# Optimization experiments

Measured on AMD Instinct MI355X. Metric: run time of the kernel, lower is better.

The kernel has to match this reference:

```python
import jax, jax.numpy as jnp
import numpy as np
import math

D_MODEL = 1024
N_HEADS = 16
HEAD_DIM = D_MODEL // N_HEADS


def get_slopes(n_heads: int) -> jnp.ndarray:
    def pow2_slopes(n):
        start = 2.0 ** (-8.0 / n)
        return np.array([start * start ** i for i in range(n)], dtype=np.float32)
    if math.log2(n_heads).is_integer():
        return jnp.asarray(pow2_slopes(n_heads))
    closest = 2 ** math.floor(math.log2(n_heads))
    base = pow2_slopes(closest)
    extra = pow2_slopes(2 * closest)[::2][: n_heads - closest]
    return jnp.asarray(np.concatenate([base, extra]))


def setup_inputs() -> dict:
    key = jax.random.key(0)
    ks = jax.random.split(key, 9)
    s = 1.0 / math.sqrt(D_MODEL)
    x = jax.random.normal(ks[0], (2, 2048, D_MODEL), dtype=jnp.float32)
    q_w = jax.random.uniform(ks[1], (D_MODEL, D_MODEL), jnp.float32, -s, s)
    q_b = jax.random.uniform(ks[2], (D_MODEL,), jnp.float32, -s, s)
    k_w = jax.random.uniform(ks[3], (D_MODEL, D_MODEL), jnp.float32, -s, s)
    k_b = jax.random.uniform(ks[4], (D_MODEL,), jnp.float32, -s, s)
    v_w = jax.random.uniform(ks[5], (D_MODEL, D_MODEL), jnp.float32, -s, s)
    v_b = jax.random.uniform(ks[6], (D_MODEL,), jnp.float32, -s, s)
    o_w = jax.random.uniform(ks[7], (D_MODEL, D_MODEL), jnp.float32, -s, s)
    o_b = jax.random.uniform(ks[8], (D_MODEL,), jnp.float32, -s, s)
    return {"x": x, "q_w": q_w, "q_b": q_b, "k_w": k_w, "k_b": k_b,
            "v_w": v_w, "v_b": v_b, "o_w": o_w, "o_b": o_b}


def reference(x, q_w, q_b, k_w, k_b, v_w, v_b, o_w, o_b):
    B, S, D = x.shape
    H, hd = N_HEADS, HEAD_DIM
    # torch Linear: y = x @ W.T + b
    Q = (x @ q_w.T + q_b).reshape(B, S, H, hd).transpose(0, 2, 1, 3)  # [B,H,S,hd]
    K = (x @ k_w.T + k_b).reshape(B, S, H, hd).transpose(0, 2, 1, 3)
    V = (x @ v_w.T + v_b).reshape(B, S, H, hd).transpose(0, 2, 1, 3)
    scores = jnp.einsum('bhqd,bhkd->bhqk', Q, K) / math.sqrt(hd)
    # ALiBi bias: slopes[h] * (k_pos - q_pos)
    pos = jnp.arange(S)
    rel = (pos[None, :] - pos[:, None]).astype(scores.dtype)  # [S,S]
    slopes = get_slopes(H)
    scores = scores + slopes[None, :, None, None] * rel[None, None, :, :]
    # causal mask
    causal = pos[None, :] <= pos[:, None]  # [S,S] True where allowed
    scores = jnp.where(causal[None, None], scores, -jnp.inf)
    attn = jax.nn.softmax(scores, axis=-1)  # dropout=0 (eval)
    out = jnp.einsum('bhqk,bhkd->bhqd', attn, V)
    out = out.transpose(0, 2, 1, 3).reshape(B, S, D)
    return out @ o_w.T + o_b
```

## Files before the change

### kernel.cpp

```cpp
#include <hip/hip_runtime.h>

typedef __attribute__((ext_vector_type(8))) short short8;
typedef __attribute__((ext_vector_type(4))) float float4v;
typedef __attribute__((ext_vector_type(4))) short short4v;

#define B_ 2
#define S_ 2048
#define D_ 1024
#define H_ 16
#define HD_ 64
#define M_ 4096
#define LOG2E 1.442695040888963f

__device__ __forceinline__ unsigned short f2bf(float f) {
  unsigned int u = __builtin_bit_cast(unsigned int, f);
  u += 0x7fffu + ((u >> 16) & 1u);
  return (unsigned short)(u >> 16);
}

__device__ __forceinline__ void gload_lds16(const void* g, void* l) {
  __builtin_amdgcn_global_load_lds(
      (const __attribute__((address_space(1))) void*)g,
      (__attribute__((address_space(3))) void*)l, 16, 0, 0);
}

__global__ __launch_bounds__(256, 4) void cvt_kernel(
    const float* __restrict__ x,  const float* __restrict__ qw,
    const float* __restrict__ kw, const float* __restrict__ vw,
    const float* __restrict__ ow, unsigned short* __restrict__ dst)
{
  const int seg = blockIdx.y;
  const float* src;
  size_t doff;
  if (seg < 4)       { src = x + (size_t)seg * 1048576; doff = (size_t)seg * 1048576; }
  else if (seg == 4) { src = qw; doff = 4194304u; }
  else if (seg == 5) { src = kw; doff = 4194304u + 1048576u; }
  else if (seg == 6) { src = vw; doff = 4194304u + 2097152u; }
  else               { src = ow; doff = 4194304u + 3145728u; }
  const size_t i = ((size_t)blockIdx.x * 256 + threadIdx.x) * 4;
  float4v v = *(const float4v*)(src + i);
  short4v p;
#pragma unroll
  for (int r = 0; r < 4; ++r) p[r] = (short)f2bf(v[r]);
  *(short4v*)(dst + doff + i) = p;
}

__global__ __launch_bounds__(256, 2) void gemm_kernel(
    const unsigned short* __restrict__ X,
    const unsigned short* __restrict__ W0, const unsigned short* __restrict__ W1,
    const unsigned short* __restrict__ W2,
    const float* __restrict__ Bi0, const float* __restrict__ Bi1,
    const float* __restrict__ Bi2,
    unsigned short* O0, unsigned short* O1, unsigned short* O2,
    float* OutF, int md0, int md1, int md2)
{
  const int z = blockIdx.z;
  const unsigned short* W  = (z == 0) ? W0  : ((z == 1) ? W1  : W2);
  const float* Bi          = (z == 0) ? Bi0 : ((z == 1) ? Bi1 : Bi2);
  unsigned short* Out      = (z == 0) ? O0  : ((z == 1) ? O1  : O2);
  const int mode           = (z == 0) ? md0 : ((z == 1) ? md1 : md2);

  __shared__ __align__(16) char smem[128 * 32 * 2 * 2];
  char* As = smem;
  char* Bs = smem + 128 * 32 * 2;

  const int t = threadIdx.x, l = t & 63;
  const int w = t >> 6, lr = l & 15, lg = l >> 4;
  const int n0 = blockIdx.x * 128, m0 = blockIdx.y * 128;
  const int wm = (w >> 1) * 64, wn = (w & 1) * 64;

  float4v acc[4][4];
#pragma unroll
  for (int i = 0; i < 4; ++i)
#pragma unroll
    for (int j = 0; j < 4; ++j) acc[i][j] = (float4v){0.f, 0.f, 0.f, 0.f};

  const int c0 = t, c1 = t + 256;
  const int r0 = c0 >> 2, k80 = (c0 & 3) * 8;
  const int r1 = c1 >> 2, k81 = (c1 & 3) * 8;

  for (int k0 = 0; k0 < 1024; k0 += 32) {
    __syncthreads();
    gload_lds16(X + (size_t)(m0 + r0) * 1024 + k0 + k80, As + c0 * 16);
    gload_lds16(X + (size_t)(m0 + r1) * 1024 + k0 + k81, As + c1 * 16);
    gload_lds16(W + (size_t)(n0 + r0) * 1024 + k0 + k80, Bs + c0 * 16);
    gload_lds16(W + (size_t)(n0 + r1) * 1024 + k0 + k81, Bs + c1 * 16);
    __syncthreads();

    short8 af[4], bfr[4];
#pragma unroll
    for (int i = 0; i < 4; ++i)
      af[i] = *(const short8*)(As + (wm + i * 16 + lr) * 64 + lg * 16);
#pragma unroll
    for (int j = 0; j < 4; ++j)
      bfr[j] = *(const short8*)(Bs + (wn + j * 16 + lr) * 64 + lg * 16);
#pragma unroll
    for (int i = 0; i < 4; ++i)
#pragma unroll
      for (int j = 0; j < 4; ++j)
        acc[i][j] = __builtin_amdgcn_mfma_f32_16x16x32_bf16(af[i], bfr[j], acc[i][j], 0, 0, 0);
  }

  float bv[4];
#pragma unroll
  for (int j = 0; j < 4; ++j) bv[j] = Bi[n0 + wn + j * 16 + lr];

#pragma unroll
  for (int i = 0; i < 4; ++i) {
    const int rowb = m0 + wm + i * 16 + lg * 4;
#pragma unroll
    for (int j = 0; j < 4; ++j) {
      const int col = n0 + wn + j * 16 + lr;
      if (mode == 2) {
        const int b = rowb >> 11, s = rowb & 2047;
        const int hh = col >> 6, d = col & 63;
        short4v pk;
#pragma unroll
        for (int r = 0; r < 4; ++r) pk[r] = (short)f2bf(acc[i][j][r] + bv[j]);
        *(short4v*)(Out + ((size_t)(b * H_ + hh) * HD_ + d) * S_ + s) = pk;
      } else if (mode == 1) {
#pragma unroll
        for (int r = 0; r < 4; ++r) {
          const int row = rowb + r;
          const int b = row >> 11, s = row & 2047;
          const int hh = col >> 6, d = col & 63;
          Out[((size_t)(b * H_ + hh) * S_ + s) * HD_ + d] = f2bf(acc[i][j][r] + bv[j]);
        }
      } else {
#pragma unroll
        for (int r = 0; r < 4; ++r)
          OutF[(size_t)(rowb + r) * 1024 + col] = acc[i][j][r] + bv[j];
      }
    }
  }
}

__global__ __launch_bounds__(256, 2) void attn_kernel(
    const unsigned short* __restrict__ Q, const unsigned short* __restrict__ K,
    const unsigned short* __restrict__ VT, unsigned short* __restrict__ O)
{
  __shared__ __align__(16) char smem[32768 + 9216];

  const int t = threadIdx.x, l = t & 63;
  const int w = t >> 6, lr = l & 15, lg = l >> 4;
  const int bh = blockIdx.x;
  const int it = 31 - (int)blockIdx.y;
  const int h = bh & 15;

  const unsigned short* qbp = Q + (size_t)bh * S_ * HD_;
  const unsigned short* kbp = K + (size_t)bh * S_ * HD_;
  const unsigned short* vbp = VT + (size_t)bh * HD_ * S_;

  const float slope2 = __builtin_amdgcn_exp2f(-0.5f * (float)(h + 1)) * LOG2E;
  const float qksc = 0.125f * LOG2E;

  char* pw = smem + 32768 + w * (16 * 144);

  short8 ones;
#pragma unroll
  for (int e = 0; e < 8; ++e) ones[e] = (short)0x3F80;

  const int g0 = t, g1 = t + 256;
  const int sr0 = g0 >> 3, sc0 = (g0 & 7) ^ (sr0 & 7);
  const int sr1 = g1 >> 3, sc1 = (g1 & 7) ^ (sr1 & 7);

  const int fchunk = ((4 + lg) ^ (lr & 7)) * 16;
  const int fchunk0 = ((lg) ^ (lr & 7)) * 16;

  const int qrow = it * 64 + w * 16;

  short8 qf[2];
#pragma unroll
  for (int ks = 0; ks < 2; ++ks)
    qf[ks] = *(const short8*)(qbp + (size_t)(qrow + lr) * HD_ + ks * 32 + lg * 8);

  float4v o_acc[4];
#pragma unroll
  for (int dt = 0; dt < 4; ++dt) o_acc[dt] = (float4v){0.f, 0.f, 0.f, 0.f};
  float m_st[4], l_st[4];
#pragma unroll
  for (int r = 0; r < 4; ++r) { m_st[r] = -1e30f; l_st[r] = 0.f; }

  gload_lds16(kbp + (size_t)sr0 * HD_ + sc0 * 8, smem + g0 * 16);
  gload_lds16(kbp + (size_t)sr1 * HD_ + sc1 * 8, smem + g1 * 16);
  gload_lds16(vbp + (size_t)sr0 * S_ + sc0 * 8, smem + 16384 + g0 * 16);
  gload_lds16(vbp + (size_t)sr1 * S_ + sc1 * 8, smem + 16384 + g1 * 16);
  __syncthreads();

  for (int j = 0; j <= it; ++j) {
    const int cur = j & 1;
    char* Ks = smem + (cur ? 8192 : 0);
    char* Vs = smem + 16384 + (cur ? 8192 : 0);
    if (j < it) {
      char* Kn = smem + (cur ? 0 : 8192);
      char* Vn = smem + 16384 + (cur ? 0 : 8192);
      const int jn = j + 1;
      gload_lds16(kbp + (size_t)(jn * 64 + sr0) * HD_ + sc0 * 8, Kn + g0 * 16);
      gload_lds16(kbp + (size_t)(jn * 64 + sr1) * HD_ + sc1 * 8, Kn + g1 * 16);
      gload_lds16(vbp + (size_t)sr0 * S_ + jn * 64 + sc0 * 8, Vn + g0 * 16);
      gload_lds16(vbp + (size_t)sr1 * S_ + jn * 64 + sc1 * 8, Vn + g1 * 16);
    }

    float4v s_acc[4];
#pragma unroll
    for (int nj = 0; nj < 4; ++nj) {
      s_acc[nj] = (float4v){0.f, 0.f, 0.f, 0.f};
      short8 kf0 = *(const short8*)(Ks + (nj * 16 + lr) * 128 + fchunk0);
      s_acc[nj] = __builtin_amdgcn_mfma_f32_16x16x32_bf16(qf[0], kf0, s_acc[nj], 0, 0, 0);
      short8 kf1 = *(const short8*)(Ks + (nj * 16 + lr) * 128 + fchunk);
      s_acc[nj] = __builtin_amdgcn_mfma_f32_16x16x32_bf16(qf[1], kf1, s_acc[nj], 0, 0, 0);
    }

    const bool domask = (j == it);
#pragma unroll
    for (int nj = 0; nj < 4; ++nj) {
      const int kpos = j * 64 + nj * 16 + lr;
      const float cb = slope2 * (float)kpos;
#pragma unroll
      for (int r = 0; r < 4; ++r) {
        float sv = s_acc[nj][r] * qksc + cb;
        if (domask && kpos > qrow + lg * 4 + r) sv = -1e30f;
        s_acc[nj][r] = sv;
      }
    }

    float ar[4];
#pragma unroll
    for (int r = 0; r < 4; ++r) {
      float mx = fmaxf(fmaxf(s_acc[0][r], s_acc[1][r]),
                       fmaxf(s_acc[2][r], s_acc[3][r]));
#pragma unroll
      for (int d = 1; d < 16; d <<= 1) mx = fmaxf(mx, __shfl_xor(mx, d, 64));
      const float mn = fmaxf(m_st[r], mx);
      ar[r] = __builtin_amdgcn_exp2f(m_st[r] - mn);
      m_st[r] = mn;
#pragma unroll
      for (int nj = 0; nj < 4; ++nj)
        s_acc[nj][r] = __builtin_amdgcn_exp2f(s_acc[nj][r] - mn);
#pragma unroll
      for (int dt = 0; dt < 4; ++dt) o_acc[dt][r] *= ar[r];
    }

#pragma unroll
    for (int nj = 0; nj < 4; ++nj)
#pragma unroll
      for (int r = 0; r < 4; ++r)
        *(unsigned short*)(pw + (lg * 4 + r) * 144 + (nj * 16 + lr) * 2) =
            f2bf(s_acc[nj][r]);

    short8 pf[2];
#pragma unroll
    for (int ks = 0; ks < 2; ++ks)
      pf[ks] = *(const short8*)(pw + lr * 144 + ks * 64 + lg * 16);

    float4v rs = (float4v){0.f, 0.f, 0.f, 0.f};
    rs = __builtin_amdgcn_mfma_f32_16x16x32_bf16(pf[0], ones, rs, 0, 0, 0);
    rs = __builtin_amdgcn_mfma_f32_16x16x32_bf16(pf[1], ones, rs, 0, 0, 0);
#pragma unroll
    for (int r = 0; r < 4; ++r) l_st[r] = ar[r] * l_st[r] + rs[r];

#pragma unroll
    for (int dt = 0; dt < 4; ++dt) {
      short8 vf0 = *(const short8*)(Vs + (dt * 16 + lr) * 128 + fchunk0);
      o_acc[dt] = __builtin_amdgcn_mfma_f32_16x16x32_bf16(pf[0], vf0, o_acc[dt], 0, 0, 0);
      short8 vf1 = *(const short8*)(Vs + (dt * 16 + lr) * 128 + fchunk);
      o_acc[dt] = __builtin_amdgcn_mfma_f32_16x16x32_bf16(pf[1], vf1, o_acc[dt], 0, 0, 0);
    }
    __syncthreads();
  }

  const int brow = (bh >> 4) * S_;
#pragma unroll
  for (int r = 0; r < 4; ++r) {
    const float inv = 1.0f / l_st[r];
    const int qp = qrow + lg * 4 + r;
#pragma unroll
    for (int dt = 0; dt < 4; ++dt)
      O[(size_t)(brow + qp) * 1024 + h * 64 + dt * 16 + lr] = f2bf(o_acc[dt][r] * inv);
  }
}

extern "C" void kernel_launch(void* const* d_in, const int* in_sizes, int n_in,
                              void* d_out, int out_size, void* d_ws, size_t ws_size,
                              hipStream_t stream) {
  (void)in_sizes; (void)n_in; (void)out_size; (void)ws_size;
  const float* x  = (const float*)d_in[0];
  const float* qw = (const float*)d_in[1];
  const float* qb = (const float*)d_in[2];
  const float* kw = (const float*)d_in[3];
  const float* kb = (const float*)d_in[4];
  const float* vw = (const float*)d_in[5];
  const float* vb = (const float*)d_in[6];
  const float* ow = (const float*)d_in[7];
  const float* ob = (const float*)d_in[8];
  float* out = (float*)d_out;

  unsigned short* xb  = (unsigned short*)d_ws;
  unsigned short* qwb = xb  + (size_t)M_ * D_;
  unsigned short* kwb = qwb + (size_t)D_ * D_;
  unsigned short* vwb = kwb + (size_t)D_ * D_;
  unsigned short* owb = vwb + (size_t)D_ * D_;
  unsigned short* qws = owb + (size_t)D_ * D_;
  unsigned short* kws = qws + (size_t)M_ * D_;
  unsigned short* vws = kws + (size_t)M_ * D_;
  unsigned short* aws = vws + (size_t)M_ * D_;

  cvt_kernel<<<dim3(1024, 8), dim3(256), 0, stream>>>(x, qw, kw, vw, ow, xb);
  gemm_kernel<<<dim3(8, 32, 3), dim3(256), 0, stream>>>(
      xb, qwb, kwb, vwb, qb, kb, vb, qws, kws, vws, out, 1, 1, 2);
  attn_kernel<<<dim3(32, 32), dim3(256), 0, stream>>>(qws, kws, vws, aws);
  gemm_kernel<<<dim3(8, 32, 1), dim3(256), 0, stream>>>(
      aws, owb, owb, owb, ob, ob, ob, aws, aws, aws, out, 0, 0, 0);
}
```

Measured before the change: 200.2 us.

## Compute transposed scores in attention to keep P in registers

New measurement: 193.3 us. 3.4% less time.

```diff
diff --git a/kernel.cpp b/kernel.cpp
--- a/kernel.cpp
+++ b/kernel.cpp
@@ -139,7 +139,7 @@
     const unsigned short* __restrict__ Q, const unsigned short* __restrict__ K,
     const unsigned short* __restrict__ VT, unsigned short* __restrict__ O)
 {
-  __shared__ __align__(16) char smem[32768 + 9216];
+  __shared__ __align__(16) char smem[32768 + 4 * 4416];
 
   const int t = threadIdx.x, l = t & 63;
   const int w = t >> 6, lr = l & 15, lg = l >> 4;
@@ -154,11 +154,7 @@
   const float slope2 = __builtin_amdgcn_exp2f(-0.5f * (float)(h + 1)) * LOG2E;
   const float qksc = 0.125f * LOG2E;
 
-  char* pw = smem + 32768 + w * (16 * 144);
-
-  short8 ones;
-#pragma unroll
-  for (int e = 0; e < 8; ++e) ones[e] = (short)0x3F80;
+  char* tw = smem + 32768 + w * 4416;
 
   const int g0 = t, g1 = t + 256;
   const int sr0 = g0 >> 3, sc0 = (g0 & 7) ^ (sr0 & 7);
@@ -168,6 +164,14 @@
   const int fchunk0 = ((lg) ^ (lr & 7)) * 16;
 
   const int qrow = it * 64 + w * 16;
+  const int qpos = qrow + lr;
+
+  float kb16[4][4];
+#pragma unroll
+  for (int nj = 0; nj < 4; ++nj)
+#pragma unroll
+    for (int r = 0; r < 4; ++r)
+      kb16[nj][r] = slope2 * (float)(nj * 16 + lg * 4 + r);
 
   short8 qf[2];
 #pragma unroll
@@ -177,9 +181,7 @@
   float4v o_acc[4];
 #pragma unroll
   for (int dt = 0; dt < 4; ++dt) o_acc[dt] = (float4v){0.f, 0.f, 0.f, 0.f};
-  float m_st[4], l_st[4];
-#pragma unroll
-  for (int r = 0; r < 4; ++r) { m_st[r] = -1e30f; l_st[r] = 0.f; }
+  float m_st = -1e30f, l_st = 0.f;
 
   gload_lds16(kbp + (size_t)sr0 * HD_ + sc0 * 8, smem + g0 * 16);
   gload_lds16(kbp + (size_t)sr1 * HD_ + sc1 * 8, smem + g1 * 16);
@@ -206,78 +208,101 @@
     for (int nj = 0; nj < 4; ++nj) {
       s_acc[nj] = (float4v){0.f, 0.f, 0.f, 0.f};
       short8 kf0 = *(const short8*)(Ks + (nj * 16 + lr) * 128 + fchunk0);
-      s_acc[nj] = __builtin_amdgcn_mfma_f32_16x16x32_bf16(qf[0], kf0, s_acc[nj], 0, 0, 0);
+      s_acc[nj] = __builtin_amdgcn_mfma_f32_16x16x32_bf16(kf0, qf[0], s_acc[nj], 0, 0, 0);
       short8 kf1 = *(const short8*)(Ks + (nj * 16 + lr) * 128 + fchunk);
-      s_acc[nj] = __builtin_amdgcn_mfma_f32_16x16x32_bf16(qf[1], kf1, s_acc[nj], 0, 0, 0);
-    }
-
-    const bool domask = (j == it);
-#pragma unroll
-    for (int nj = 0; nj < 4; ++nj) {
-      const int kpos = j * 64 + nj * 16 + lr;
-      const float cb = slope2 * (float)kpos;
+      s_acc[nj] = __builtin_amdgcn_mfma_f32_16x16x32_bf16(kf1, qf[1], s_acc[nj], 0, 0, 0);
+    }
+
+    const float cj = slope2 * (float)(j * 64);
+#pragma unroll
+    for (int nj = 0; nj < 4; ++nj)
+#pragma unroll
+      for (int r = 0; r < 4; ++r)
+        s_acc[nj][r] = s_acc[nj][r] * qksc + (cj + kb16[nj][r]);
+    if (j == it) {
+#pragma unroll
+      for (int nj = 0; nj < 4; ++nj)
+#pragma unroll
+        for (int r = 0; r < 4; ++r) {
+          const int kpos = j * 64 + nj * 16 + lg * 4 + r;
+          if (kpos > qpos) s_acc[nj][r] = -1e30f;
+        }
+    }
+
+    float mx = s_acc[0][0];
+#pragma unroll
+    for (int nj = 0; nj < 4; ++nj)
+#pragma unroll
+      for (int r = 0; r < 4; ++r) mx = fmaxf(mx, s_acc[nj][r]);
+    mx = fmaxf(mx, __shfl_xor(mx, 16, 64));
+    mx = fmaxf(mx, __shfl_xor(mx, 32, 64));
+    const float mn = fmaxf(m_st, mx);
+    const float alpha = __builtin_amdgcn_exp2f(m_st - mn);
+    m_st = mn;
+    float rsum = 0.f;
+#pragma unroll
+    for (int nj = 0; nj < 4; ++nj)
 #pragma unroll
       for (int r = 0; r < 4; ++r) {
-        float sv = s_acc[nj][r] * qksc + cb;
-        if (domask && kpos > qrow + lg * 4 + r) sv = -1e30f;
-        s_acc[nj][r] = sv;
+        const float p = __builtin_amdgcn_exp2f(s_acc[nj][r] - mn);
+        s_acc[nj][r] = p;
+        rsum += p;
       }
-    }
-
-    float ar[4];
-#pragma unroll
-    for (int r = 0; r < 4; ++r) {
-      float mx = fmaxf(fmaxf(s_acc[0][r], s_acc[1][r]),
-                       fmaxf(s_acc[2][r], s_acc[3][r]));
-#pragma unroll
-      for (int d = 1; d < 16; d <<= 1) mx = fmaxf(mx, __shfl_xor(mx, d, 64));
-      const float mn = fmaxf(m_st[r], mx);
-      ar[r] = __builtin_amdgcn_exp2f(m_st[r] - mn);
-      m_st[r] = mn;
-#pragma unroll
-      for (int nj = 0; nj < 4; ++nj)
-        s_acc[nj][r] = __builtin_amdgcn_exp2f(s_acc[nj][r] - mn);
-#pragma unroll
-      for (int dt = 0; dt < 4; ++dt) o_acc[dt][r] *= ar[r];
-    }
-
-#pragma unroll
-    for (int nj = 0; nj < 4; ++nj)
-#pragma unroll
-      for (int r = 0; r < 4; ++r)
-        *(unsigned short*)(pw + (lg * 4 + r) * 144 + (nj * 16 + lr) * 2) =
-            f2bf(s_acc[nj][r]);
-
-    short8 pf[2];
-#pragma unroll
-    for (int ks = 0; ks < 2; ++ks)
-      pf[ks] = *(const short8*)(pw + lr * 144 + ks * 64 + lg * 16);
-
-    float4v rs = (float4v){0.f, 0.f, 0.f, 0.f};
-    rs = __builtin_amdgcn_mfma_f32_16x16x32_bf16(pf[0], ones, rs, 0, 0, 0);
-    rs = __builtin_amdgcn_mfma_f32_16x16x32_bf16(pf[1], ones, rs, 0, 0, 0);
-#pragma unroll
-    for (int r = 0; r < 4; ++r) l_st[r] = ar[r] * l_st[r] + rs[r];
-
+    rsum += __shfl_xor(rsum, 16, 64);
+    rsum += __shfl_xor(rsum, 32, 64);
+    l_st = alpha * l_st + rsum;
+#pragma unroll
+    for (int dt = 0; dt < 4; ++dt)
+#pragma unroll
+      for (int r = 0; r < 4; ++r) o_acc[dt][r] *= alpha;
+
+    short8 pT[2];
+#pragma unroll
+    for (int njp = 0; njp < 2; ++njp)
+#pragma unroll
+      for (int jj = 0; jj < 4; ++jj) {
+        pT[njp][jj]     = (short)f2bf(s_acc[njp * 2][jj]);
+        pT[njp][jj + 4] = (short)f2bf(s_acc[njp * 2 + 1][jj]);
+      }
+
+    const int vcl = lr & 7;
 #pragma unroll
     for (int dt = 0; dt < 4; ++dt) {
-      short8 vf0 = *(const short8*)(Vs + (dt * 16 + lr) * 128 + fchunk0);
-      o_acc[dt] = __builtin_amdgcn_mfma_f32_16x16x32_bf16(pf[0], vf0, o_acc[dt], 0, 0, 0);
-      short8 vf1 = *(const short8*)(Vs + (dt * 16 + lr) * 128 + fchunk);
-      o_acc[dt] = __builtin_amdgcn_mfma_f32_16x16x32_bf16(pf[1], vf1, o_acc[dt], 0, 0, 0);
+      const char* rowp = Vs + (dt * 16 + lr) * 128;
+#pragma unroll
+      for (int njp = 0; njp < 2; ++njp) {
+        const int cA = ((njp * 4 + (lg >> 1)) ^ vcl) * 16 + (lg & 1) * 8;
+        const int cB = ((njp * 4 + 2 + (lg >> 1)) ^ vcl) * 16 + (lg & 1) * 8;
+        short4v v0 = *(const short4v*)(rowp + cA);
+        short4v v1 = *(const short4v*)(rowp + cB);
+        short8 vf8;
+#pragma unroll
+        for (int e = 0; e < 4; ++e) { vf8[e] = v0[e]; vf8[e + 4] = v1[e]; }
+        o_acc[dt] = __builtin_amdgcn_mfma_f32_16x16x32_bf16(vf8, pT[njp], o_acc[dt], 0, 0, 0);
+      }
     }
     __syncthreads();
   }
 
+#pragma unroll
+  for (int dt = 0; dt < 4; ++dt)
+#pragma unroll
+    for (int r = 0; r < 4; ++r)
+      *(float*)(tw + ((dt * 16 + lg * 4 + r) * 17 + lr) * 4) = o_acc[dt][r];
+  if (lg == 0) *(float*)(tw + 4352 + lr * 4) = l_st;
+
+  const int q2 = l >> 2, dbase = (l & 3) * 16;
+  const float invl = 1.0f / *(const float*)(tw + 4352 + q2 * 4);
+  short8 os[2];
+#pragma unroll
+  for (int i = 0; i < 16; ++i) {
+    const float v = *(const float*)(tw + ((dbase + i) * 17 + q2) * 4) * invl;
+    os[i >> 3][i & 7] = (short)f2bf(v);
+  }
   const int brow = (bh >> 4) * S_;
-#pragma unroll
-  for (int r = 0; r < 4; ++r) {
-    const float inv = 1.0f / l_st[r];
-    const int qp = qrow + lg * 4 + r;
-#pragma unroll
-    for (int dt = 0; dt < 4; ++dt)
-      O[(size_t)(brow + qp) * 1024 + h * 64 + dt * 16 + lr] = f2bf(o_acc[dt][r] * inv);
-  }
+  unsigned short* op = O + (size_t)(brow + qrow + q2) * 1024 + h * 64 + dbase;
+  *(short8*)op = os[0];
+  *(short8*)(op + 8) = os[1];
 }
 
 extern "C" void kernel_launch(void* const* d_in, const int* in_sizes, int n_in,
```
